# Performance work log

Measured on AMD Instinct MI355X. Metric: run time of the kernel, lower is better.

## Reference

```python
import jax, jax.numpy as jnp
import numpy as np

N_NODES = 10000
W_DIM = 512
N_EDGES = 200000


def setup_inputs() -> dict:
    key = jax.random.key(0)
    k1, k2, k3 = jax.random.split(key, 3)
    z_drug = jax.random.normal(k1, (N_NODES, W_DIM), dtype=jnp.float32)
    # glorot-style init for the bilinear weight
    glorot_std = jnp.sqrt(2.0 / (W_DIM + W_DIM)).astype(jnp.float32)
    weight = jax.random.normal(k2, (W_DIM, W_DIM), dtype=jnp.float32) * glorot_std
    batch_edges = jax.random.randint(k3, (2, N_EDGES), 0, N_NODES, dtype=jnp.int64)
    return {"z_drug": z_drug, "weight": weight, "batch_edges": batch_edges}


def reference(z_drug, weight, batch_edges):
    # edge_type == 'drug_drug': both endpoints come from the drug table.
    row_embed = z_drug[batch_edges[0]]  # [E, d]
    col_embed = z_drug[batch_edges[1]]  # [E, d]
    # score_e = row_e @ W @ col_e  == diag((Z1 W) Z2^T) without the N x N blowup
    score = jnp.einsum('ed,df,ef->e', row_embed, weight, col_embed)
    return jax.nn.sigmoid(score)  # is_sigmoid=True default
```

## Files before the change

kernel.cpp:

```cpp
#include <hip/hip_runtime.h>
#include <math.h>

#define DIM     512
#define NNODES  10000
#define NEDGES  200000
#define MPAD    10048
#define NMB     157
#define NGRP    5
#define NB      (NGRP * NNODES)
#define SCAN_N  49
#define GEMM_GRID (NMB * 4)

#define HIST_BLK   50
#define SCAN_BASE  50
#define SCAT_BASE  99
#define SCAT_N     98
#define GEMM_BASE  197
#define FUSE_GRID  (GEMM_BASE + GEMM_GRID)

using floatx4 = __attribute__((ext_vector_type(4))) float;
using half8   = __attribute__((ext_vector_type(8))) _Float16;
using half2v  = __attribute__((ext_vector_type(2))) _Float16;

__device__ inline float dot2acc(half2v a, half2v b, float c) {
#if __has_builtin(__builtin_amdgcn_fdot2)
    return __builtin_amdgcn_fdot2(a, b, c, false);
#else
    return fmaf((float)a[0], (float)b[0], fmaf((float)a[1], (float)b[1], c));
#endif
}

__device__ inline int aload(const int* p) {
    return __hip_atomic_load(p, __ATOMIC_RELAXED, __HIP_MEMORY_SCOPE_AGENT);
}
__device__ inline void astore(int* p, int v) {
    __hip_atomic_store(p, v, __ATOMIC_RELAXED, __HIP_MEMORY_SCOPE_AGENT);
}
__device__ inline void waitflag(int* f, int target) {
    while (__hip_atomic_load(f, __ATOMIC_RELAXED, __HIP_MEMORY_SCOPE_AGENT) < target)
        __builtin_amdgcn_s_sleep(8);
    __atomic_signal_fence(__ATOMIC_ACQUIRE);
}
__device__ inline void signal(int* f) {
    __atomic_signal_fence(__ATOMIC_RELEASE);
    __hip_atomic_fetch_add(f, 1, __ATOMIC_RELAXED, __HIP_MEMORY_SCOPE_AGENT);
}

#define PREP_ZBLK 2512
__global__ __launch_bounds__(256) void prep(const float* __restrict__ Z,
                                            const float* __restrict__ W,
                                            _Float16* __restrict__ Zh16,
                                            _Float16* __restrict__ Wh16t,
                                            int* __restrict__ counts,
                                            int* __restrict__ flags) {
    const int b = blockIdx.x;
    const int t = threadIdx.x;

    if (b == 0 && t < 4) flags[t] = 0;

    if (b < 196) {
        int i = b * 256 + t;
        if (i < NB) counts[i] = 0;
    }

    if (b < PREP_ZBLK) {
        const int idx8 = (b * 256 + t) * 8;
        const int m = idx8 >> 9;
        float x[8];
        if (m < NNODES) {
            float4 v0 = *(const float4*)(Z + idx8);
            float4 v1 = *(const float4*)(Z + idx8 + 4);
            x[0]=v0.x; x[1]=v0.y; x[2]=v0.z; x[3]=v0.w;
            x[4]=v1.x; x[5]=v1.y; x[6]=v1.z; x[7]=v1.w;
        } else {
            #pragma unroll
            for (int j = 0; j < 8; ++j) x[j] = 0.f;
        }
        half8 h;
        #pragma unroll
        for (int j = 0; j < 8; ++j) h[j] = (_Float16)x[j];
        *(half8*)(Zh16 + idx8) = h;
    } else {
        __shared__ float tile[64][65];
        const int wb = b - PREP_ZBLK;
        const int kb = (wb >> 3) * 64;
        const int nb = (wb & 7) * 64;
        const int kk = t >> 2;
        const int ch = t & 3;

        const float* src = W + (size_t)(kb + kk) * DIM + nb + ch * 16;
        #pragma unroll
        for (int q = 0; q < 4; ++q) {
            float4 v = *(const float4*)(src + q * 4);
            tile[kk][ch * 16 + q * 4 + 0] = v.x;
            tile[kk][ch * 16 + q * 4 + 1] = v.y;
            tile[kk][ch * 16 + q * 4 + 2] = v.z;
            tile[kk][ch * 16 + q * 4 + 3] = v.w;
        }
        __syncthreads();

        const int nn = kk;
        half8 h0, h1;
        #pragma unroll
        for (int i = 0; i < 8; ++i) h0[i] = (_Float16)tile[ch * 16 + i][nn];
        #pragma unroll
        for (int i = 0; i < 8; ++i) h1[i] = (_Float16)tile[ch * 16 + 8 + i][nn];
        _Float16* d = Wh16t + (size_t)(nb + nn) * DIM + kb + ch * 16;
        *(half8*)(d)     = h0;
        *(half8*)(d + 8) = h1;
    }
}

__global__ __launch_bounds__(256, 4) void gemm_sort(
        const _Float16* __restrict__ Zh16,
        const _Float16* __restrict__ Wh16t,
        _Float16* __restrict__ ZWh,
        const int* __restrict__ eidx,
        int* __restrict__ counts,
        int* __restrict__ cursor,
        int* __restrict__ blksum,
        unsigned* __restrict__ keys,
        unsigned short* __restrict__ rows16,
        int* __restrict__ flags)
{
    __shared__ int wsum[4];
    __shared__ int sbase;

    const int t   = threadIdx.x;
    const int bid = blockIdx.x;

    if (bid >= GEMM_BASE) {
        const int vb  = bid - GEMM_BASE;
        const int m0  = (vb >> 2) * 64;
        const int n0w = (vb & 3) * 128 + (t >> 6) * 32;

        const int l  = t & 63;
        const int lm = l & 15;
        const int lq = l >> 4;

        const _Float16* pa0 = Zh16 + (size_t)(m0 + lm) * DIM + lq * 8;
        const _Float16* pa1 = pa0 + (size_t)16 * DIM;
        const _Float16* pa2 = pa0 + (size_t)32 * DIM;
        const _Float16* pa3 = pa0 + (size_t)48 * DIM;
        const _Float16* pb0 = Wh16t + (size_t)(n0w + lm) * DIM + lq * 8;
        const _Float16* pb1 = pb0 + (size_t)16 * DIM;

        floatx4 acc[4][2] = {};

        #pragma unroll
        for (int s = 0; s < 16; ++s) {
            const int off = s * 32;
            half8 a0 = *(const half8*)(pa0 + off);
            half8 a1 = *(const half8*)(pa1 + off);
            half8 a2 = *(const half8*)(pa2 + off);
            half8 a3 = *(const half8*)(pa3 + off);
            half8 b0 = *(const half8*)(pb0 + off);
            half8 b1 = *(const half8*)(pb1 + off);

            acc[0][0] = __builtin_amdgcn_mfma_f32_16x16x32_f16(a0, b0, acc[0][0], 0, 0, 0);
            acc[0][1] = __builtin_amdgcn_mfma_f32_16x16x32_f16(a0, b1, acc[0][1], 0, 0, 0);
            acc[1][0] = __builtin_amdgcn_mfma_f32_16x16x32_f16(a1, b0, acc[1][0], 0, 0, 0);
            acc[1][1] = __builtin_amdgcn_mfma_f32_16x16x32_f16(a1, b1, acc[1][1], 0, 0, 0);
            acc[2][0] = __builtin_amdgcn_mfma_f32_16x16x32_f16(a2, b0, acc[2][0], 0, 0, 0);
            acc[2][1] = __builtin_amdgcn_mfma_f32_16x16x32_f16(a2, b1, acc[2][1], 0, 0, 0);
            acc[3][0] = __builtin_amdgcn_mfma_f32_16x16x32_f16(a3, b0, acc[3][0], 0, 0, 0);
            acc[3][1] = __builtin_amdgcn_mfma_f32_16x16x32_f16(a3, b1, acc[3][1], 0, 0, 0);
        }

        #pragma unroll
        for (int i = 0; i < 4; ++i)
            #pragma unroll
            for (int j = 0; j < 2; ++j)
                #pragma unroll
                for (int r = 0; r < 4; ++r) {
                    const int gm = m0 + 16 * i + lq * 4 + r;
                    const int gn = n0w + 16 * j + lm;
                    if (gm < NNODES)
                        ZWh[(size_t)gm * DIM + gn] = (_Float16)acc[i][j][r];
                }
        return;
    }

    if (bid < HIST_BLK) {
        for (int e = bid * 256 + t; e < NEDGES; e += HIST_BLK * 256) {
            int r = eidx[e];
            int c = eidx[NEDGES + e];
            atomicAdd(&counts[(c >> 11) * NNODES + r], 1);
        }
        __syncthreads();
        if (t == 0) signal(&flags[0]);
        return;
    }

    if (bid < SCAT_BASE) {
        const int b = bid - SCAN_BASE;
        const int lane = t & 63;
        const int wv   = t >> 6;

        if (t == 0) waitflag(&flags[0], HIST_BLK);
        __syncthreads();

        const int base = b * 1024 + t * 4;
        int v0 = 0, v1 = 0, v2 = 0, v3 = 0;
        if (base + 3 < NB) {
            v0 = aload(counts + base);
            v1 = aload(counts + base + 1);
            v2 = aload(counts + base + 2);
            v3 = aload(counts + base + 3);
        } else {
            if (base     < NB) v0 = aload(counts + base);
            if (base + 1 < NB) v1 = aload(counts + base + 1);
            if (base + 2 < NB) v2 = aload(counts + base + 2);
        }
        const int ts = v0 + v1 + v2 + v3;
        int incl = ts;
        #pragma unroll
        for (int off = 1; off < 64; off <<= 1) {
            int u = __shfl_up(incl, off, 64);
            if (lane >= off) incl += u;
        }
        if (lane == 63) wsum[wv] = incl;
        __syncthreads();
        int wb = 0;
        #pragma unroll
        for (int k = 0; k < 4; ++k) if (k < wv) wb += wsum[k];
        const int ex   = wb + incl - ts;
        const int pre0 = ex;
        const int pre1 = ex + v0;
        const int pre2 = pre1 + v1;
        const int pre3 = pre2 + v2;
        if (t == 255) astore(blksum + b, wb + incl);
        __syncthreads();
        if (t == 0) { signal(&flags[1]); waitflag(&flags[1], SCAN_N); }
        __syncthreads();

        if (t < 64) {
            int v = (t < b) ? aload(blksum + t) : 0;
            #pragma unroll
            for (int off = 32; off > 0; off >>= 1)
                v += __shfl_xor(v, off, 64);
            if (t == 0) sbase = v;
        }
        __syncthreads();
        const int b0 = sbase;

        if (base + 3 < NB) {
            astore(cursor + base,     b0 + pre0);
            astore(cursor + base + 1, b0 + pre1);
            astore(cursor + base + 2, b0 + pre2);
            astore(cursor + base + 3, b0 + pre3);
        } else {
            if (base     < NB) astore(cursor + base,     b0 + pre0);
            if (base + 1 < NB) astore(cursor + base + 1, b0 + pre1);
            if (base + 2 < NB) astore(cursor + base + 2, b0 + pre2);
        }
        __syncthreads();
        if (t == 0) signal(&flags[2]);
        return;
    }

    {
        if (t == 0) waitflag(&flags[2], SCAN_N);
        __syncthreads();

        for (int e = (bid - SCAT_BASE) * 256 + t; e < NEDGES; e += SCAT_N * 256) {
            int r = eidx[e];
            int c = eidx[NEDGES + e];
            int pos = atomicAdd(&cursor[(c >> 11) * NNODES + r], 1);
            keys[pos]   = ((unsigned)c << 18) | (unsigned)e;
            rows16[pos] = (unsigned short)r;
        }
    }
}

__global__ __launch_bounds__(256) void edge_score_f(const _Float16* __restrict__ ZWh,
                                                    const _Float16* __restrict__ Zh,
                                                    const unsigned* __restrict__ keys,
                                                    const unsigned short* __restrict__ rows16,
                                                    float* __restrict__ out) {
    const int t    = threadIdx.x;
    const int wgid = blockIdx.x * 4 + (t >> 6);
    const int lane = t & 63;
    const int gq   = lane >> 4;
    const int sl   = lane & 15;

    const int ii = wgid * 4 + gq;
    const unsigned k = keys[ii];
    const int c = (int)(k >> 18);
    const int r = (int)rows16[ii];

    const _Float16* rp = ZWh + (size_t)r * DIM + sl * 32;
    const _Float16* cp = Zh  + (size_t)c * DIM + sl * 32;

    half8 ra0 = *(const half8*)(rp);
    half8 ra1 = *(const half8*)(rp + 8);
    half8 ra2 = *(const half8*)(rp + 16);
    half8 ra3 = *(const half8*)(rp + 24);
    half8 c0  = *(const half8*)(cp);
    half8 c1  = *(const half8*)(cp + 8);
    half8 c2  = *(const half8*)(cp + 16);
    half8 c3  = *(const half8*)(cp + 24);

    float s = 0.f;
    #pragma unroll
    for (int d = 0; d < 4; ++d) {
        s = dot2acc((half2v){ra0[2*d], ra0[2*d+1]}, (half2v){c0[2*d], c0[2*d+1]}, s);
        s = dot2acc((half2v){ra1[2*d], ra1[2*d+1]}, (half2v){c1[2*d], c1[2*d+1]}, s);
        s = dot2acc((half2v){ra2[2*d], ra2[2*d+1]}, (half2v){c2[2*d], c2[2*d+1]}, s);
        s = dot2acc((half2v){ra3[2*d], ra3[2*d+1]}, (half2v){c3[2*d], c3[2*d+1]}, s);
    }

    s += __shfl_xor(s, 1, 64);
    s += __shfl_xor(s, 2, 64);
    s += __shfl_xor(s, 4, 64);
    s += __shfl_xor(s, 8, 64);

    if (sl == 0)
        out[k & 0x3FFFFu] = 1.0f / (1.0f + expf(-s));
}

#define GTM 128
#define GTN 64
#define GTK 16
#define LDA 132
#define LDB 68

__global__ __launch_bounds__(256) void gemm_zw(const float* __restrict__ A,
                                               const float* __restrict__ B,
                                               float* __restrict__ C) {
    __shared__ float As[GTK * LDA];
    __shared__ float Bs[GTK * LDB];

    const int t  = threadIdx.x;
    const int m0 = blockIdx.x * GTM;
    const int n0 = blockIdx.y * GTN;
    const int tx = t & 15;
    const int ty = t >> 4;

    float acc[8][4] = {};

    for (int k0 = 0; k0 < DIM; k0 += GTK) {
        #pragma unroll
        for (int p = 0; p < 2; ++p) {
            int f  = t + p * 256;
            int mm = f >> 2;
            int kq = f & 3;
            int m  = m0 + mm;
            float4 v = make_float4(0.f, 0.f, 0.f, 0.f);
            if (m < NNODES)
                v = *(const float4*)(A + (size_t)m * DIM + k0 + kq * 4);
            As[(kq * 4 + 0) * LDA + mm] = v.x;
            As[(kq * 4 + 1) * LDA + mm] = v.y;
            As[(kq * 4 + 2) * LDA + mm] = v.z;
            As[(kq * 4 + 3) * LDA + mm] = v.w;
        }
        {
            int kb = t >> 4, n4 = t & 15;
            *(float4*)&Bs[kb * LDB + n4 * 4] =
                *(const float4*)(B + (size_t)(k0 + kb) * DIM + n0 + n4 * 4);
        }
        __syncthreads();

        #pragma unroll
        for (int kk = 0; kk < GTK; ++kk) {
            float4 a0 = *(const float4*)&As[kk * LDA + ty * 8];
            float4 a1 = *(const float4*)&As[kk * LDA + ty * 8 + 4];
            float4 b  = *(const float4*)&Bs[kk * LDB + tx * 4];
            float av[8] = {a0.x, a0.y, a0.z, a0.w, a1.x, a1.y, a1.z, a1.w};
            float bv[4] = {b.x, b.y, b.z, b.w};
            #pragma unroll
            for (int i = 0; i < 8; ++i)
                #pragma unroll
                for (int j = 0; j < 4; ++j)
                    acc[i][j] = fmaf(av[i], bv[j], acc[i][j]);
        }
        __syncthreads();
    }

    #pragma unroll
    for (int i = 0; i < 8; ++i) {
        int m = m0 + ty * 8 + i;
        if (m < NNODES)
            *(float4*)(C + (size_t)m * DIM + n0 + tx * 4) =
                make_float4(acc[i][0], acc[i][1], acc[i][2], acc[i][3]);
    }
}

__global__ __launch_bounds__(256) void edge_score(const float* __restrict__ ZW,
                                                  const float* __restrict__ Z,
                                                  const int* __restrict__ eidx,
                                                  float* __restrict__ out) {
    const int e    = blockIdx.x * 4 + (threadIdx.x >> 6);
    const int lane = threadIdx.x & 63;

    const int r = eidx[e];
    const int c = eidx[NEDGES + e];

    const float4* pr = (const float4*)(ZW + (size_t)r * DIM);
    const float4* pc = (const float4*)(Z  + (size_t)c * DIM);

    float4 a0 = pr[lane * 2 + 0];
    float4 a1 = pr[lane * 2 + 1];
    float4 b0 = pc[lane * 2 + 0];
    float4 b1 = pc[lane * 2 + 1];

    float s = a0.x * b0.x;
    s = fmaf(a0.y, b0.y, s);
    s = fmaf(a0.z, b0.z, s);
    s = fmaf(a0.w, b0.w, s);
    s = fmaf(a1.x, b1.x, s);
    s = fmaf(a1.y, b1.y, s);
    s = fmaf(a1.z, b1.z, s);
    s = fmaf(a1.w, b1.w, s);

    #pragma unroll
    for (int off = 32; off > 0; off >>= 1)
        s += __shfl_xor(s, off, 64);

    if (lane == 0)
        out[e] = 1.0f / (1.0f + expf(-s));
}

extern "C" void kernel_launch(void* const* d_in, const int* in_sizes, int n_in,
                              void* d_out, int out_size, void* d_ws, size_t ws_size,
                              hipStream_t stream) {
    const float* Z  = (const float*)d_in[0];
    const float* W  = (const float*)d_in[1];
    const int*   EI = (const int*)d_in[2];
    float* out = (float*)d_out;

    char* p = (char*)d_ws;
    _Float16* ZWh   = (_Float16*)p;  p += (size_t)MPAD * DIM * 2;
    _Float16* Zh16  = (_Float16*)p;  p += (size_t)MPAD * DIM * 2;
    _Float16* Wh16t = (_Float16*)p;  p += (size_t)DIM * DIM * 2;
    int* counts  = (int*)p;          p += (size_t)NB * 4;
    int* cursor  = (int*)p;          p += (size_t)NB * 4;
    int* blksum  = (int*)p;          p += (size_t)SCAN_N * 4;
    unsigned* keys = (unsigned*)p;   p += (size_t)NEDGES * 4;
    unsigned short* rows16 = (unsigned short*)p; p += (size_t)NEDGES * 2;
    int* flags = (int*)p;            p += 4 * 4;
    const size_t need_full = (size_t)(p - (char*)d_ws);

    if (ws_size >= need_full) {
        prep<<<PREP_ZBLK + 64, 256, 0, stream>>>(Z, W, Zh16, Wh16t, counts, flags);
        gemm_sort<<<FUSE_GRID, 256, 0, stream>>>(Zh16, Wh16t, ZWh, EI, counts,
                                                 cursor, blksum, keys, rows16, flags);
        edge_score_f<<<NEDGES / 16, 256, 0, stream>>>(ZWh, Zh16, keys, rows16, out);
    } else {
        float* ZW = (float*)d_ws;
        dim3 g1((NNODES + GTM - 1) / GTM, DIM / GTN);
        gemm_zw<<<g1, 256, 0, stream>>>(Z, W, ZW);
        edge_score<<<NEDGES / 4, 256, 0, stream>>>(ZW, Z, EI, out);
    }
}
```

Measured before the change: 149.2 us.

## Shrink GEMM warp tiles to 32x32 with 64x64 block tiles and triple-buffered loads

```diff
diff --git a/kernel.cpp b/kernel.cpp
--- a/kernel.cpp
+++ b/kernel.cpp
@@ -9,7 +9,7 @@
 #define NGRP    5
 #define NB      (NGRP * NNODES)
 #define SCAN_N  49
-#define GEMM_GRID (NMB * 4)
+#define GEMM_GRID (NMB * 8)
 
 #define HIST_BLK   50
 #define SCAN_BASE  50
@@ -130,51 +130,53 @@
     const int bid = blockIdx.x;
 
     if (bid >= GEMM_BASE) {
-        const int vb  = bid - GEMM_BASE;
-        const int m0  = (vb >> 2) * 64;
-        const int n0w = (vb & 3) * 128 + (t >> 6) * 32;
-
+        const int vb = bid - GEMM_BASE;
+        const int w  = t >> 6;
         const int l  = t & 63;
         const int lm = l & 15;
         const int lq = l >> 4;
+        const int m0 = (vb >> 3) * 64 + (w & 1) * 32;
+        const int n0 = (vb & 7) * 64 + (w >> 1) * 32;
 
         const _Float16* pa0 = Zh16 + (size_t)(m0 + lm) * DIM + lq * 8;
         const _Float16* pa1 = pa0 + (size_t)16 * DIM;
-        const _Float16* pa2 = pa0 + (size_t)32 * DIM;
-        const _Float16* pa3 = pa0 + (size_t)48 * DIM;
-        const _Float16* pb0 = Wh16t + (size_t)(n0w + lm) * DIM + lq * 8;
+        const _Float16* pb0 = Wh16t + (size_t)(n0 + lm) * DIM + lq * 8;
         const _Float16* pb1 = pb0 + (size_t)16 * DIM;
 
-        floatx4 acc[4][2] = {};
+        floatx4 acc[2][2] = {};
+        half8 A0[3], A1[3], B0[3], B1[3];
+
+#define GLOAD(slot, step) do {                                   \
+            A0[slot] = *(const half8*)(pa0 + (step) * 32);       \
+            A1[slot] = *(const half8*)(pa1 + (step) * 32);       \
+            B0[slot] = *(const half8*)(pb0 + (step) * 32);       \
+            B1[slot] = *(const half8*)(pb1 + (step) * 32); } while (0)
+
+        GLOAD(0, 0);
+        GLOAD(1, 1);
 
         #pragma unroll
         for (int s = 0; s < 16; ++s) {
-            const int off = s * 32;
-            half8 a0 = *(const half8*)(pa0 + off);
-            half8 a1 = *(const half8*)(pa1 + off);
-            half8 a2 = *(const half8*)(pa2 + off);
-            half8 a3 = *(const half8*)(pa3 + off);
-            half8 b0 = *(const half8*)(pb0 + off);
-            half8 b1 = *(const half8*)(pb1 + off);
-
-            acc[0][0] = __builtin_amdgcn_mfma_f32_16x16x32_f16(a0, b0, acc[0][0], 0, 0, 0);
-            acc[0][1] = __builtin_amdgcn_mfma_f32_16x16x32_f16(a0, b1, acc[0][1], 0, 0, 0);
-            acc[1][0] = __builtin_amdgcn_mfma_f32_16x16x32_f16(a1, b0, acc[1][0], 0, 0, 0);
-            acc[1][1] = __builtin_amdgcn_mfma_f32_16x16x32_f16(a1, b1, acc[1][1], 0, 0, 0);
-            acc[2][0] = __builtin_amdgcn_mfma_f32_16x16x32_f16(a2, b0, acc[2][0], 0, 0, 0);
-            acc[2][1] = __builtin_amdgcn_mfma_f32_16x16x32_f16(a2, b1, acc[2][1], 0, 0, 0);
-            acc[3][0] = __builtin_amdgcn_mfma_f32_16x16x32_f16(a3, b0, acc[3][0], 0, 0, 0);
-            acc[3][1] = __builtin_amdgcn_mfma_f32_16x16x32_f16(a3, b1, acc[3][1], 0, 0, 0);
-        }
-
-        #pragma unroll
-        for (int i = 0; i < 4; ++i)
+            const int cur = s % 3;
+            if (s < 14) {
+                const int nx = (s + 2) % 3;
+                GLOAD(nx, s + 2);
+            }
+            acc[0][0] = __builtin_amdgcn_mfma_f32_16x16x32_f16(A0[cur], B0[cur], acc[0][0], 0, 0, 0);
+            acc[0][1] = __builtin_amdgcn_mfma_f32_16x16x32_f16(A0[cur], B1[cur], acc[0][1], 0, 0, 0);
+            acc[1][0] = __builtin_amdgcn_mfma_f32_16x16x32_f16(A1[cur], B0[cur], acc[1][0], 0, 0, 0);
+            acc[1][1] = __builtin_amdgcn_mfma_f32_16x16x32_f16(A1[cur], B1[cur], acc[1][1], 0, 0, 0);
+        }
+#undef GLOAD
+
+        #pragma unroll
+        for (int i = 0; i < 2; ++i)
             #pragma unroll
             for (int j = 0; j < 2; ++j)
                 #pragma unroll
                 for (int r = 0; r < 4; ++r) {
                     const int gm = m0 + 16 * i + lq * 4 + r;
-                    const int gn = n0w + 16 * j + lm;
+                    const int gn = n0 + 16 * j + lm;
                     if (gm < NNODES)
                         ZWh[(size_t)gm * DIM + gn] = (_Float16)acc[i][j][r];
                 }
```

Result: slower. 162.6 us (+8.9%).
